# Optimization experiments

Hardware: AMD Instinct MI355X
Metric: run time of the kernel (lower is better)

## Reference

```python
import math
import jax, jax.numpy as jnp
import numpy as np

W_SIZE = 7
NUM_HEADS = 12


def _shift_masks(w: int, d: int):
    # upper/lower mask (applied to last row of windows)
    ul = np.zeros((w * w, w * w), np.float32)
    ul[-d * w:, :-d * w] = -np.inf
    ul[:-d * w, -d * w:] = -np.inf
    # left/right mask (applied to last column of windows)
    lr = np.zeros((w, w, w, w), np.float32)
    lr[:, -d:, :, :-d] = -np.inf
    lr[:, :-d, :, -d:] = -np.inf
    lr = lr.reshape(w * w, w * w)
    return jnp.asarray(ul), jnp.asarray(lr)


def _rel_pos_index(w: int):
    # standard Swin relative-position index, shape (w*w, w*w), values in [0, (2w-1)^2)
    coords = np.stack(np.meshgrid(np.arange(w), np.arange(w), indexing='ij'), 0).reshape(2, -1)  # (2, w*w)
    rel = coords[:, :, None] - coords[:, None, :]  # (2, ww, ww)
    idx = (rel[0] + w - 1) * (2 * w - 1) + (rel[1] + w - 1)
    return jnp.asarray(idx, dtype=jnp.int32)


def setup_inputs() -> dict:
    key = jax.random.key(0)
    ks = jax.random.split(key, 6)
    E, w = 384, W_SIZE
    return {
        'x': jax.random.normal(ks[0], (32, 56, 56, E), jnp.float32),
        'w_qkv': jax.random.normal(ks[1], (3 * E, E), jnp.float32) * 0.02,
        'b_qkv': jax.random.normal(ks[2], (3 * E,), jnp.float32) * 0.02,
        'w_proj': jax.random.normal(ks[3], (E, E), jnp.float32) * 0.02,
        'b_proj': jax.random.normal(ks[4], (E,), jnp.float32) * 0.02,
        'rel_table': jax.random.normal(ks[5], ((2 * w - 1) ** 2, NUM_HEADS), jnp.float32) * 0.02,
    }


def reference(x, w_qkv, b_qkv, w_proj, b_proj, rel_table):
    w = W_SIZE
    heads = NUM_HEADS
    B, H, Wd, C = x.shape
    hd = C // heads
    nh, nw, ww = H // w, Wd // w, w * w

    # shift (matches torch roll(shifts=(-w//2, -w//2)) == -4 for w=7)
    x = jnp.roll(x, ((-w) // 2, (-w) // 2), axis=(1, 2))

    # window partition: (B, nh, nw, ww, C)
    xw = x.reshape(B, nh, w, nw, w, C).transpose(0, 1, 3, 2, 4, 5).reshape(B, nh, nw, ww, C)

    qkv = xw @ w_qkv.T + b_qkv  # (B, nh, nw, ww, 3C)
    q, k, v = jnp.split(qkv, 3, axis=-1)

    def heads_first(t):  # (B, nh, nw, heads, ww, hd)
        return t.reshape(B, nh, nw, ww, heads, hd).transpose(0, 1, 2, 4, 3, 5)

    q, k, v = heads_first(q), heads_first(k), heads_first(v)

    attn = jnp.einsum('bhwnqd,bhwnkd->bhwnqk', q, k) * (1.0 / math.sqrt(hd))

    # relative position bias: (heads, ww, ww)
    bias = rel_table[_rel_pos_index(w)].transpose(2, 0, 1)
    attn = attn + bias

    # shift masks on last row / last column of windows
    ul, lr = _shift_masks(w, w // 2)
    mask = jnp.zeros((nh, nw, 1, ww, ww), attn.dtype)
    mask = mask.at[-1].add(ul)
    mask = mask.at[:, -1].add(lr)
    attn = attn + mask

    p = jax.nn.softmax(attn, axis=-1)
    o = jnp.einsum('bhwnqk,bhwnkd->bhwnqd', p, v)  # (B, nh, nw, heads, ww, hd)

    # merge heads and un-window
    o = o.transpose(0, 1, 2, 4, 3, 5).reshape(B, nh, nw, w, w, C)
    o = o.transpose(0, 1, 3, 2, 4, 5).reshape(B, H, Wd, C)

    o = jnp.roll(o, (w // 2, w // 2), axis=(1, 2))
    return o @ w_proj.T + b_proj
```

## Files before the change

kernel.cpp:

```cpp
#include <hip/hip_runtime.h>
#include <hip/hip_bf16.h>


typedef __bf16 bf16x8 __attribute__((ext_vector_type(8)));
typedef float  floatx4 __attribute__((ext_vector_type(4)));
typedef short  short8  __attribute__((ext_vector_type(8)));

#define MFMA16(a, b, c) __builtin_amdgcn_mfma_f32_16x16x32_bf16((a), (b), (c), 0, 0, 0)

static __device__ __forceinline__ int src_off(int gm) {
  int win = gm / 49, t = gm - win * 49;
  int b = win >> 6, rr = win & 63;
  int wi = rr >> 3, wj = rr & 7;
  int ty = t / 7, tx = t - ty * 7;
  int y = wi * 7 + ty + 4; if (y >= 56) y -= 56;
  int x = wj * 7 + tx + 4; if (x >= 56) x -= 56;
  return ((b * 56 + y) * 56 + x) * 384;
}

static __device__ __forceinline__ int dst_off(int gm) {
  int win = gm / 49, t = gm - win * 49;
  int b = win >> 6, rr = win & 63;
  int wi = rr >> 3, wj = rr & 7;
  int ty = t / 7, tx = t - ty * 7;
  int y = wi * 7 + ty + 3; if (y >= 56) y -= 56;
  int x = wj * 7 + tx + 3; if (x >= 56) x -= 56;
  return ((b * 56 + y) * 56 + x) * 384;
}

static __device__ __forceinline__ float bf_lo(unsigned u) {
  union { unsigned v; float f; } c; c.v = u << 16; return c.f;
}
static __device__ __forceinline__ float bf_hi(unsigned u) {
  union { unsigned v; float f; } c; c.v = u & 0xFFFF0000u; return c.f;
}

__global__ __launch_bounds__(256) void prep_kernel(
    const float* __restrict__ w_qkv, const float* __restrict__ w_proj,
    const float* __restrict__ rel_table,
    __hip_bfloat16* __restrict__ wqkv_bf, __hip_bfloat16* __restrict__ wproj_bf,
    __hip_bfloat16* __restrict__ bias2) {
  const int N1 = 3 * 384 * 384;
  const int N2 = 384 * 384;
  const int N3 = 12 * 4 * 4 * 64 * 4;
  int i = blockIdx.x * 256 + threadIdx.x;
  if (i < N1) wqkv_bf[i] = __float2bfloat16(w_qkv[i]);
  int j = i - N1;
  if (j >= 0 && j < N2) wproj_bf[j] = __float2bfloat16(w_proj[j]);
  int k = i - N1 - N2;
  if (k >= 0 && k < N3) {
    int r = k & 3;
    int lp = (k >> 2) & 63;
    int ni = (k >> 8) & 3;
    int mi = (k >> 10) & 3;
    int head = k >> 12;
    int m = mi * 16 + (lp & 15);
    int n = ni * 16 + (lp >> 4) * 4 + r;
    float val = -1e30f;
    if (m < 49 && n < 49) {
      int dy = m / 7 - n / 7 + 6;
      int dx = m % 7 - n % 7 + 6;
      val = rel_table[(dy * 13 + dx) * 12 + head];
    }
    bias2[k] = __float2bfloat16(val);
  }
}

__global__ __launch_bounds__(768, 3) void mega_kernel(
    const float* __restrict__ x, const __hip_bfloat16* __restrict__ wq,
    const float* __restrict__ bqkv, const __hip_bfloat16* __restrict__ bias2,
    const __hip_bfloat16* __restrict__ wp, const float* __restrict__ bproj,
    __hip_bfloat16* __restrict__ vt, float* __restrict__ out) {
  __shared__ __hip_bfloat16 xo_lds[49][392];
  __shared__ __hip_bfloat16 q_lds[49][392];
  __shared__ __hip_bfloat16 k_lds[49][392];
  __shared__ __hip_bfloat16 p_lds[12][16][64];

  int blk = blockIdx.x;
  int win = (blk & 7) * 256 + (blk >> 3);
  int tid = threadIdx.x;
  int wv = tid >> 6, l = tid & 63;
  int g = l >> 4, q16 = l & 15;
  const int sw = q16 & 7;

  floatx4 zc;
  zc[0] = zc[1] = zc[2] = zc[3] = 0.f;

  for (int i = tid; i < 49 * 48; i += 768) {
    int row = i / 48, c8 = (i - row * 48) * 8;
    int so = src_off(win * 49 + row) + c8;
    floatx4 a = *(const floatx4*)(x + so);
    floatx4 b = *(const floatx4*)(x + so + 4);
    union { __hip_bfloat16 h[8]; short8 s; } u;
#pragma unroll
    for (int e = 0; e < 4; ++e) {
      u.h[e]     = __float2bfloat16(a[e]);
      u.h[4 + e] = __float2bfloat16(b[e]);
    }
    *(short8*)&xo_lds[row][c8] = u.s;
  }
  __syncthreads();

  {
    const bool isv = (wv >= 8);
    const bool isq = (wv < 4);
    __hip_bfloat16* dst = isq ? &q_lds[0][0] : &k_lds[0][0];
#pragma unroll 2
    for (int pass = 0; pass < 2; ++pass) {
      int n0 = wv * 96 + pass * 48;
      floatx4 acc[12];
#pragma unroll
      for (int i = 0; i < 12; ++i) acc[i] = zc;

#pragma unroll
      for (int ks = 0; ks < 12; ++ks) {
        int k0 = ks * 32;
        bf16x8 af[4], bf[3];
#pragma unroll
        for (int mi = 0; mi < 4; ++mi) {
          int row = mi * 16 + q16;
          row = row < 49 ? row : 48;
          af[mi] = *(const bf16x8*)&xo_lds[row][k0 + g * 8];
        }
#pragma unroll
        for (int ni = 0; ni < 3; ++ni)
          bf[ni] = *(const bf16x8*)(wq + (size_t)(n0 + ni * 16 + q16) * 384 + k0 + g * 8);
        __builtin_amdgcn_s_setprio(1);
        if (!isv) {
#pragma unroll
          for (int mi = 0; mi < 4; ++mi)
#pragma unroll
            for (int ni = 0; ni < 3; ++ni)
              acc[mi * 3 + ni] = MFMA16(af[mi], bf[ni], acc[mi * 3 + ni]);
        } else {
#pragma unroll
          for (int ai = 0; ai < 3; ++ai)
#pragma unroll
            for (int bj = 0; bj < 4; ++bj)
              acc[ai * 4 + bj] = MFMA16(bf[ai], af[bj], acc[ai * 4 + bj]);
        }
        __builtin_amdgcn_s_setprio(0);
      }

      if (!isv) {
#pragma unroll
        for (int ni = 0; ni < 3; ++ni) {
          int n = n0 + ni * 16 + q16;
          float bn = bqkv[n];
          int nn = isq ? n : (n - 384);
#pragma unroll
          for (int mi = 0; mi < 4; ++mi) {
#pragma unroll
            for (int r = 0; r < 4; ++r) {
              int m = mi * 16 + g * 4 + r;
              if (m < 49) {
                float v = acc[mi * 3 + ni][r] + bn;
                if (isq) v *= 0.17677669529663687f;
                dst[m * 392 + nn] = __float2bfloat16(v);
              }
            }
          }
        }
      } else {
#pragma unroll
        for (int ai = 0; ai < 3; ++ai) {
#pragma unroll
          for (int r = 0; r < 4; ++r) {
            int n = n0 + ai * 16 + g * 4 + r;
            float bn = bqkv[n];
            int d = n - 768;
#pragma unroll
            for (int bj = 0; bj < 4; ++bj) {
              int t = bj * 16 + q16;
              vt[((size_t)win * 384 + d) * 64 + t] =
                  __float2bfloat16(acc[ai * 4 + bj][r] + bn);
            }
          }
        }
      }
    }
  }
  __syncthreads();

  {
    const int head = wv;
    int wr = win & 63;
    const bool lastrow = ((wr >> 3) == 7);
    const bool lastcol = ((wr & 7) == 7);

    unsigned long long badbits = 0ull;
    if (lastrow || lastcol) {
#pragma unroll
      for (int mi = 0; mi < 4; ++mi) {
        int m = mi * 16 + q16;
        int m7 = m % 7;
        bool m28 = (m >= 28), m74 = (m7 >= 4);
#pragma unroll
        for (int ni = 0; ni < 4; ++ni) {
#pragma unroll
          for (int r = 0; r < 4; ++r) {
            int n = ni * 16 + g * 4 + r;
            bool bad = (lastrow && (m28 != (n >= 28))) ||
                       (lastcol && (m74 != ((n % 7) >= 4)));
            if (bad) badbits |= (1ull << (mi * 16 + ni * 4 + r));
          }
        }
      }
    }

    bf16x8 aq[4], bk[4];
#pragma unroll
    for (int mi = 0; mi < 4; ++mi) {
      int row = mi * 16 + q16;
      row = row < 49 ? row : 48;
      aq[mi] = *(const bf16x8*)&q_lds[row][head * 32 + g * 8];
      bk[mi] = *(const bf16x8*)&k_lds[row][head * 32 + g * 8];
    }

    floatx4 st[4][4];
    __builtin_amdgcn_s_setprio(1);
#pragma unroll
    for (int ni = 0; ni < 4; ++ni)
#pragma unroll
      for (int mi = 0; mi < 4; ++mi)
        st[ni][mi] = MFMA16(bk[ni], aq[mi], zc);
    __builtin_amdgcn_s_setprio(0);

    const __hip_bfloat16* vp = vt + ((size_t)win * 384 + head * 32) * 64;
    bf16x8 bv[2][2];
#pragma unroll
    for (int ks = 0; ks < 2; ++ks)
#pragma unroll
      for (int n2 = 0; n2 < 2; ++n2)
        bv[ks][n2] = *(const bf16x8*)(vp + (n2 * 16 + q16) * 64 + ks * 32 + g * 8);

    const __hip_bfloat16* b2 = bias2 + (size_t)head * 4096;
    __hip_bfloat16* pw = &p_lds[wv][0][0];

#pragma unroll
    for (int mi = 0; mi < 4; ++mi) {
      uint2 braw[4];
#pragma unroll
      for (int ni = 0; ni < 4; ++ni)
        braw[ni] = *(const uint2*)(b2 + ((mi * 4 + ni) * 64 + l) * 4);

      float vals[4][4];
      float mx = -1e30f;
#pragma unroll
      for (int ni = 0; ni < 4; ++ni) {
#pragma unroll
        for (int r = 0; r < 4; ++r) {
          float bb = (r == 0) ? bf_lo(braw[ni].x) : (r == 1) ? bf_hi(braw[ni].x)
                     : (r == 2) ? bf_lo(braw[ni].y) : bf_hi(braw[ni].y);
          float v = st[ni][mi][r] + bb;
          if ((badbits >> (mi * 16 + ni * 4 + r)) & 1) v = -1e30f;
          vals[ni][r] = v;
          mx = fmaxf(mx, v);
        }
      }
      mx = fmaxf(mx, __shfl_xor(mx, 16));
      mx = fmaxf(mx, __shfl_xor(mx, 32));
      float sum = 0.f;
#pragma unroll
      for (int ni = 0; ni < 4; ++ni) {
#pragma unroll
        for (int r = 0; r < 4; ++r) {
          float p = __expf(vals[ni][r] - mx);
          vals[ni][r] = p;
          sum += p;
        }
      }
      sum += __shfl_xor(sum, 16);
      sum += __shfl_xor(sum, 32);
      float inv = 1.0f / sum;

#pragma unroll
      for (int ni = 0; ni < 4; ++ni) {
        union { __hip_bfloat16 h[4]; unsigned long long u; } pk;
#pragma unroll
        for (int r = 0; r < 4; ++r) pk.h[r] = __float2bfloat16(vals[ni][r] * inv);
        int pc = (2 * ni + (g >> 1)) ^ sw;
        *(unsigned long long*)(pw + q16 * 64 + pc * 8 + (g & 1) * 4) = pk.u;
      }

      bf16x8 av0 = *(const bf16x8*)(pw + q16 * 64 + (g ^ sw) * 8);
      bf16x8 av1 = *(const bf16x8*)(pw + q16 * 64 + ((4 + g) ^ sw) * 8);
      floatx4 o2[2];
      o2[0] = o2[1] = zc;
#pragma unroll
      for (int n2 = 0; n2 < 2; ++n2) {
        o2[n2] = MFMA16(av0, bv[0][n2], o2[n2]);
        o2[n2] = MFMA16(av1, bv[1][n2], o2[n2]);
      }
#pragma unroll
      for (int r = 0; r < 4; ++r) {
        int m = mi * 16 + g * 4 + r;
        if (m < 49) {
#pragma unroll
          for (int n2 = 0; n2 < 2; ++n2)
            xo_lds[m][head * 32 + n2 * 16 + q16] = __float2bfloat16(o2[n2][r]);
        }
      }
    }
  }
  __syncthreads();

  {
    floatx4 pacc[4][2];
#pragma unroll
    for (int i = 0; i < 4; ++i)
#pragma unroll
      for (int j = 0; j < 2; ++j) pacc[i][j] = zc;

    for (int k0 = 0; k0 < 384; k0 += 32) {
      bf16x8 af[4], bfr[2];
#pragma unroll
      for (int mi = 0; mi < 4; ++mi) {
        int row = mi * 16 + q16;
        row = row < 49 ? row : 48;
        af[mi] = *(const bf16x8*)&xo_lds[row][k0 + g * 8];
      }
#pragma unroll
      for (int ni = 0; ni < 2; ++ni) {
        int brow = wv * 32 + ni * 16 + q16;
        bfr[ni] = *(const bf16x8*)(wp + (size_t)brow * 384 + k0 + g * 8);
      }
      __builtin_amdgcn_s_setprio(1);
#pragma unroll
      for (int mi = 0; mi < 4; ++mi)
#pragma unroll
        for (int ni = 0; ni < 2; ++ni)
          pacc[mi][ni] = MFMA16(af[mi], bfr[ni], pacc[mi][ni]);
      __builtin_amdgcn_s_setprio(0);
    }

#pragma unroll
    for (int mi = 0; mi < 4; ++mi) {
#pragma unroll
      for (int r = 0; r < 4; ++r) {
        int m = mi * 16 + g * 4 + r;
        if (m < 49) {
          int off = dst_off(win * 49 + m);
#pragma unroll
          for (int ni = 0; ni < 2; ++ni) {
            int n = wv * 32 + ni * 16 + q16;
            out[off + n] = pacc[mi][ni][r] + bproj[n];
          }
        }
      }
    }
  }
}

extern "C" void kernel_launch(void* const* d_in, const int* in_sizes, int n_in,
                              void* d_out, int out_size, void* d_ws, size_t ws_size,
                              hipStream_t stream) {
  const float* x         = (const float*)d_in[0];
  const float* w_qkv     = (const float*)d_in[1];
  const float* b_qkv     = (const float*)d_in[2];
  const float* w_proj    = (const float*)d_in[3];
  const float* b_proj    = (const float*)d_in[4];
  const float* rel_table = (const float*)d_in[5];
  float* out = (float*)d_out;

  char* ws = (char*)d_ws;
  const size_t OFF_WQKV  = 0;
  const size_t OFF_WPROJ = 884736;
  const size_t OFF_BIAS2 = 1179648;
  const size_t OFF_VT    = 1572864;

  __hip_bfloat16* wqkv_bf  = (__hip_bfloat16*)(ws + OFF_WQKV);
  __hip_bfloat16* wproj_bf = (__hip_bfloat16*)(ws + OFF_WPROJ);
  __hip_bfloat16* bias2    = (__hip_bfloat16*)(ws + OFF_BIAS2);
  __hip_bfloat16* vt       = (__hip_bfloat16*)(ws + OFF_VT);


  prep_kernel<<<3072, 256, 0, stream>>>(w_qkv, w_proj, rel_table, wqkv_bf, wproj_bf, bias2);
  mega_kernel<<<2048, 768, 0, stream>>>(x, wqkv_bf, b_qkv, bias2, wproj_bf, b_proj, vt, out);
}
```

Measured before the change: 399.9 us.

## Compute per-head QKV in registers and keep V in LDS instead of global

Each wave now computes the Q, K and V projections for its own head rather than a slice of the fused QKV output columns. Q and K fragments are rearranged into MFMA operand layout with lane shuffles and stay in registers, so the q/k LDS buffers and one block barrier go away. V is written to a per-wave LDS buffer instead of a global scratch array, which removes a global write and read round trip. The block also holds separate x and o LDS buffers, so shared-memory use and register pressure change, and this may reduce occupancy.

```diff
diff --git a/kernel.cpp b/kernel.cpp
--- a/kernel.cpp
+++ b/kernel.cpp
@@ -5,6 +5,7 @@
 typedef __bf16 bf16x8 __attribute__((ext_vector_type(8)));
 typedef float  floatx4 __attribute__((ext_vector_type(4)));
 typedef short  short8  __attribute__((ext_vector_type(8)));
+typedef unsigned long long u64;
 
 #define MFMA16(a, b, c) __builtin_amdgcn_mfma_f32_16x16x32_bf16((a), (b), (c), 0, 0, 0)
 
@@ -70,10 +71,10 @@
     const float* __restrict__ x, const __hip_bfloat16* __restrict__ wq,
     const float* __restrict__ bqkv, const __hip_bfloat16* __restrict__ bias2,
     const __hip_bfloat16* __restrict__ wp, const float* __restrict__ bproj,
-    __hip_bfloat16* __restrict__ vt, float* __restrict__ out) {
-  __shared__ __hip_bfloat16 xo_lds[49][392];
-  __shared__ __hip_bfloat16 q_lds[49][392];
-  __shared__ __hip_bfloat16 k_lds[49][392];
+    float* __restrict__ out) {
+  __shared__ __hip_bfloat16 x_lds[49][392];
+  __shared__ __hip_bfloat16 o_lds[49][392];
+  __shared__ __hip_bfloat16 v_lds[12][32][72];
   __shared__ __hip_bfloat16 p_lds[12][16][64];
 
   int blk = blockIdx.x;
@@ -81,6 +82,7 @@
   int tid = threadIdx.x;
   int wv = tid >> 6, l = tid & 63;
   int g = l >> 4, q16 = l & 15;
+  const int head = wv;
   const int sw = q16 & 7;
 
   floatx4 zc;
@@ -97,97 +99,134 @@
       u.h[e]     = __float2bfloat16(a[e]);
       u.h[4 + e] = __float2bfloat16(b[e]);
     }
-    *(short8*)&xo_lds[row][c8] = u.s;
+    *(short8*)&x_lds[row][c8] = u.s;
   }
   __syncthreads();
 
+  floatx4 qk[4][4];
+#pragma unroll
+  for (int i = 0; i < 4; ++i)
+#pragma unroll
+    for (int j = 0; j < 4; ++j) qk[i][j] = zc;
+
+  const int rq = head * 32;
+  const int rk = 384 + head * 32;
+  const int rv = 768 + head * 32;
+
+#pragma unroll
+  for (int ks = 0; ks < 12; ++ks) {
+    int k0 = ks * 32;
+    bf16x8 af[4], wf[4];
+#pragma unroll
+    for (int bj = 0; bj < 4; ++bj) {
+      int row = bj * 16 + q16;
+      row = row < 49 ? row : 48;
+      af[bj] = *(const bf16x8*)&x_lds[row][k0 + g * 8];
+    }
+    wf[0] = *(const bf16x8*)(wq + (size_t)(rq + q16) * 384 + k0 + g * 8);
+    wf[1] = *(const bf16x8*)(wq + (size_t)(rq + 16 + q16) * 384 + k0 + g * 8);
+    wf[2] = *(const bf16x8*)(wq + (size_t)(rk + q16) * 384 + k0 + g * 8);
+    wf[3] = *(const bf16x8*)(wq + (size_t)(rk + 16 + q16) * 384 + k0 + g * 8);
+    __builtin_amdgcn_s_setprio(1);
+#pragma unroll
+    for (int ai = 0; ai < 4; ++ai)
+#pragma unroll
+      for (int bj = 0; bj < 4; ++bj)
+        qk[ai][bj] = MFMA16(wf[ai], af[bj], qk[ai][bj]);
+    __builtin_amdgcn_s_setprio(0);
+  }
+
+  floatx4 bq0 = *(const floatx4*)(bqkv + rq + g * 4);
+  floatx4 bq1 = *(const floatx4*)(bqkv + rq + 16 + g * 4);
+  floatx4 bk0 = *(const floatx4*)(bqkv + rk + g * 4);
+  floatx4 bk1 = *(const floatx4*)(bqkv + rk + 16 + g * 4);
+  const float SCALE = 0.17677669529663687f;
+  u64 pq[2][4], pk_[2][4];
+#pragma unroll
+  for (int ah = 0; ah < 2; ++ah) {
+#pragma unroll
+    for (int bj = 0; bj < 4; ++bj) {
+      union { __hip_bfloat16 h[4]; u64 u; } u1, u2;
+#pragma unroll
+      for (int r = 0; r < 4; ++r) {
+        float bqv = (ah == 0) ? bq0[r] : bq1[r];
+        float bkv = (ah == 0) ? bk0[r] : bk1[r];
+        u1.h[r] = __float2bfloat16((qk[ah][bj][r] + bqv) * SCALE);
+        u2.h[r] = __float2bfloat16(qk[2 + ah][bj][r] + bkv);
+      }
+      pq[ah][bj] = u1.u;
+      pk_[ah][bj] = u2.u;
+    }
+  }
+
+  bf16x8 aq[4], bk[4];
+#pragma unroll
+  for (int bj = 0; bj < 4; ++bj) {
+#pragma unroll
+    for (int op = 0; op < 2; ++op) {
+      u64 A  = op ? pk_[0][bj] : pq[0][bj];
+      u64 A3 = op ? pk_[1][bj] : pq[1][bj];
+      u64 B16 = __shfl_xor(A, 16);
+      u64 B32 = __shfl_xor(A, 32);
+      u64 B48 = __shfl_xor(A, 48);
+      u64 C16 = __shfl_xor(A3, 16);
+      u64 C32 = __shfl_xor(A3, 32);
+      u64 C48 = __shfl_xor(A3, 48);
+      u64 lo = (g == 0) ? A : (g == 1) ? B48 : (g == 2) ? C32 : C16;
+      u64 hi = (g == 0) ? B16 : (g == 1) ? B32 : (g == 2) ? C48 : A3;
+      union { u64 w[2]; bf16x8 v; } cb;
+      cb.w[0] = lo; cb.w[1] = hi;
+      if (op == 0) aq[bj] = cb.v; else bk[bj] = cb.v;
+    }
+  }
+
   {
-    const bool isv = (wv >= 8);
-    const bool isq = (wv < 4);
-    __hip_bfloat16* dst = isq ? &q_lds[0][0] : &k_lds[0][0];
-#pragma unroll 2
-    for (int pass = 0; pass < 2; ++pass) {
-      int n0 = wv * 96 + pass * 48;
-      floatx4 acc[12];
-#pragma unroll
-      for (int i = 0; i < 12; ++i) acc[i] = zc;
-
-#pragma unroll
-      for (int ks = 0; ks < 12; ++ks) {
-        int k0 = ks * 32;
-        bf16x8 af[4], bf[3];
-#pragma unroll
-        for (int mi = 0; mi < 4; ++mi) {
-          int row = mi * 16 + q16;
-          row = row < 49 ? row : 48;
-          af[mi] = *(const bf16x8*)&xo_lds[row][k0 + g * 8];
-        }
-#pragma unroll
-        for (int ni = 0; ni < 3; ++ni)
-          bf[ni] = *(const bf16x8*)(wq + (size_t)(n0 + ni * 16 + q16) * 384 + k0 + g * 8);
-        __builtin_amdgcn_s_setprio(1);
-        if (!isv) {
-#pragma unroll
-          for (int mi = 0; mi < 4; ++mi)
-#pragma unroll
-            for (int ni = 0; ni < 3; ++ni)
-              acc[mi * 3 + ni] = MFMA16(af[mi], bf[ni], acc[mi * 3 + ni]);
-        } else {
-#pragma unroll
-          for (int ai = 0; ai < 3; ++ai)
-#pragma unroll
-            for (int bj = 0; bj < 4; ++bj)
-              acc[ai * 4 + bj] = MFMA16(bf[ai], af[bj], acc[ai * 4 + bj]);
-        }
-        __builtin_amdgcn_s_setprio(0);
-      }
-
-      if (!isv) {
-#pragma unroll
-        for (int ni = 0; ni < 3; ++ni) {
-          int n = n0 + ni * 16 + q16;
-          float bn = bqkv[n];
-          int nn = isq ? n : (n - 384);
-#pragma unroll
-          for (int mi = 0; mi < 4; ++mi) {
-#pragma unroll
-            for (int r = 0; r < 4; ++r) {
-              int m = mi * 16 + g * 4 + r;
-              if (m < 49) {
-                float v = acc[mi * 3 + ni][r] + bn;
-                if (isq) v *= 0.17677669529663687f;
-                dst[m * 392 + nn] = __float2bfloat16(v);
-              }
-            }
-          }
-        }
-      } else {
-#pragma unroll
-        for (int ai = 0; ai < 3; ++ai) {
-#pragma unroll
-          for (int r = 0; r < 4; ++r) {
-            int n = n0 + ai * 16 + g * 4 + r;
-            float bn = bqkv[n];
-            int d = n - 768;
-#pragma unroll
-            for (int bj = 0; bj < 4; ++bj) {
-              int t = bj * 16 + q16;
-              vt[((size_t)win * 384 + d) * 64 + t] =
-                  __float2bfloat16(acc[ai * 4 + bj][r] + bn);
-            }
-          }
-        }
-      }
-    }
-  }
-  __syncthreads();
+    floatx4 av_[2][4];
+#pragma unroll
+    for (int i = 0; i < 2; ++i)
+#pragma unroll
+      for (int j = 0; j < 4; ++j) av_[i][j] = zc;
+#pragma unroll
+    for (int ks = 0; ks < 12; ++ks) {
+      int k0 = ks * 32;
+      bf16x8 af[4], wf[2];
+#pragma unroll
+      for (int bj = 0; bj < 4; ++bj) {
+        int row = bj * 16 + q16;
+        row = row < 49 ? row : 48;
+        af[bj] = *(const bf16x8*)&x_lds[row][k0 + g * 8];
+      }
+      wf[0] = *(const bf16x8*)(wq + (size_t)(rv + q16) * 384 + k0 + g * 8);
+      wf[1] = *(const bf16x8*)(wq + (size_t)(rv + 16 + q16) * 384 + k0 + g * 8);
+      __builtin_amdgcn_s_setprio(1);
+#pragma unroll
+      for (int ai = 0; ai < 2; ++ai)
+#pragma unroll
+        for (int bj = 0; bj < 4; ++bj)
+          av_[ai][bj] = MFMA16(wf[ai], af[bj], av_[ai][bj]);
+      __builtin_amdgcn_s_setprio(0);
+    }
+    floatx4 bv0 = *(const floatx4*)(bqkv + rv + g * 4);
+    floatx4 bv1 = *(const floatx4*)(bqkv + rv + 16 + g * 4);
+#pragma unroll
+    for (int ai = 0; ai < 2; ++ai) {
+#pragma unroll
+      for (int bj = 0; bj < 4; ++bj) {
+#pragma unroll
+        for (int r = 0; r < 4; ++r) {
+          int d = ai * 16 + g * 4 + r;
+          int t = bj * 16 + q16;
+          float bv = (ai == 0) ? bv0[r] : bv1[r];
+          v_lds[wv][d][t] = __float2bfloat16(av_[ai][bj][r] + bv);
+        }
+      }
+    }
+  }
 
   {
-    const int head = wv;
     int wr = win & 63;
     const bool lastrow = ((wr >> 3) == 7);
     const bool lastcol = ((wr & 7) == 7);
-
     unsigned long long badbits = 0ull;
     if (lastrow || lastcol) {
 #pragma unroll
@@ -208,15 +247,6 @@
       }
     }
 
-    bf16x8 aq[4], bk[4];
-#pragma unroll
-    for (int mi = 0; mi < 4; ++mi) {
-      int row = mi * 16 + q16;
-      row = row < 49 ? row : 48;
-      aq[mi] = *(const bf16x8*)&q_lds[row][head * 32 + g * 8];
-      bk[mi] = *(const bf16x8*)&k_lds[row][head * 32 + g * 8];
-    }
-
     floatx4 st[4][4];
     __builtin_amdgcn_s_setprio(1);
 #pragma unroll
@@ -225,14 +255,6 @@
       for (int mi = 0; mi < 4; ++mi)
         st[ni][mi] = MFMA16(bk[ni], aq[mi], zc);
     __builtin_amdgcn_s_setprio(0);
-
-    const __hip_bfloat16* vp = vt + ((size_t)win * 384 + head * 32) * 64;
-    bf16x8 bv[2][2];
-#pragma unroll
-    for (int ks = 0; ks < 2; ++ks)
-#pragma unroll
-      for (int n2 = 0; n2 < 2; ++n2)
-        bv[ks][n2] = *(const bf16x8*)(vp + (n2 * 16 + q16) * 64 + ks * 32 + g * 8);
 
     const __hip_bfloat16* b2 = bias2 + (size_t)head * 4096;
     __hip_bfloat16* pw = &p_lds[wv][0][0];
@@ -276,11 +298,11 @@
 
 #pragma unroll
       for (int ni = 0; ni < 4; ++ni) {
-        union { __hip_bfloat16 h[4]; unsigned long long u; } pk;
-#pragma unroll
-        for (int r = 0; r < 4; ++r) pk.h[r] = __float2bfloat16(vals[ni][r] * inv);
+        union { __hip_bfloat16 h[4]; u64 u; } pk2;
+#pragma unroll
+        for (int r = 0; r < 4; ++r) pk2.h[r] = __float2bfloat16(vals[ni][r] * inv);
         int pc = (2 * ni + (g >> 1)) ^ sw;
-        *(unsigned long long*)(pw + q16 * 64 + pc * 8 + (g & 1) * 4) = pk.u;
+        *(u64*)(pw + q16 * 64 + pc * 8 + (g & 1) * 4) = pk2.u;
       }
 
       bf16x8 av0 = *(const bf16x8*)(pw + q16 * 64 + (g ^ sw) * 8);
@@ -289,8 +311,10 @@
       o2[0] = o2[1] = zc;
 #pragma unroll
       for (int n2 = 0; n2 < 2; ++n2) {
-        o2[n2] = MFMA16(av0, bv[0][n2], o2[n2]);
-        o2[n2] = MFMA16(av1, bv[1][n2], o2[n2]);
+        bf16x8 bv0 = *(const bf16x8*)&v_lds[wv][n2 * 16 + q16][g * 8];
+        bf16x8 bv1 = *(const bf16x8*)&v_lds[wv][n2 * 16 + q16][32 + g * 8];
+        o2[n2] = MFMA16(av0, bv0, o2[n2]);
+        o2[n2] = MFMA16(av1, bv1, o2[n2]);
       }
 #pragma unroll
       for (int r = 0; r < 4; ++r) {
@@ -298,7 +322,7 @@
         if (m < 49) {
 #pragma unroll
           for (int n2 = 0; n2 < 2; ++n2)
-            xo_lds[m][head * 32 + n2 * 16 + q16] = __float2bfloat16(o2[n2][r]);
+            o_lds[m][head * 32 + n2 * 16 + q16] = __float2bfloat16(o2[n2][r]);
         }
       }
     }
@@ -318,7 +342,7 @@
       for (int mi = 0; mi < 4; ++mi) {
         int row = mi * 16 + q16;
         row = row < 49 ? row : 48;
-        af[mi] = *(const bf16x8*)&xo_lds[row][k0 + g * 8];
+        af[mi] = *(const bf16x8*)&o_lds[row][k0 + g * 8];
       }
 #pragma unroll
       for (int ni = 0; ni < 2; ++ni) {
@@ -367,14 +391,11 @@
   const size_t OFF_WQKV  = 0;
   const size_t OFF_WPROJ = 884736;
   const size_t OFF_BIAS2 = 1179648;
-  const size_t OFF_VT    = 1572864;
 
   __hip_bfloat16* wqkv_bf  = (__hip_bfloat16*)(ws + OFF_WQKV);
   __hip_bfloat16* wproj_bf = (__hip_bfloat16*)(ws + OFF_WPROJ);
   __hip_bfloat16* bias2    = (__hip_bfloat16*)(ws + OFF_BIAS2);
-  __hip_bfloat16* vt       = (__hip_bfloat16*)(ws + OFF_VT);
-
 
   prep_kernel<<<3072, 256, 0, stream>>>(w_qkv, w_proj, rel_table, wqkv_bf, wproj_bf, bias2);
-  mega_kernel<<<2048, 768, 0, stream>>>(x, wqkv_bf, b_qkv, bias2, wproj_bf, b_proj, vt, out);
-}
+  mega_kernel<<<2048, 768, 0, stream>>>(x, wqkv_bf, b_qkv, bias2, wproj_bf, b_proj, out);
+}
```

New measurement: 466.3 us. 16.6% more time.
